# Optimization experiments

Measured on AMD Instinct MI355X. Metric: run time of the kernel, lower is better.

The kernel has to match this reference:

```python
import jax, jax.numpy as jnp
import numpy as np

N = 8192          # total samples = n_ways * num_instances
D = 512           # embedding dim
NUM_INSTANCES = 8 # shots per class
MARGIN = 0.3
W = 1.0
EPS = 1e-12


def setup_inputs() -> dict:
    key = jax.random.key(0)
    inputs = jax.random.normal(key, (N, D), dtype=jnp.float32)
    # targets[i] = class id; classes are contiguous blocks of NUM_INSTANCES
    targets = jnp.arange(N, dtype=jnp.int32) // NUM_INSTANCES
    return {"inputs": inputs, "targets": targets}


def _pairwise_euclid(a, b):
    # sqrt(clamp(||a||^2 + ||b||^2 - 2 a.b, eps)) -- same as torch addmm path
    sq_a = jnp.sum(a * a, axis=1)          # [na]
    sq_b = jnp.sum(b * b, axis=1)          # [nb]
    d2 = sq_a[:, None] + sq_b[None, :] - 2.0 * (a @ b.T)
    return jnp.sqrt(jnp.clip(d2, EPS, None))


def reference(inputs, targets):
    n = inputs.shape[0]
    n_ways = n // NUM_INSTANCES

    dist = _pairwise_euclid(inputs, inputs)              # [n, n]
    mask = targets[:, None] == targets[None, :]          # same-class mask

    # batch-hard mining: hardest positive (max same-class dist),
    # hardest negative (min different-class dist), fully vectorized
    dist_ap = jnp.max(jnp.where(mask, dist, -jnp.inf), axis=1)  # [n]
    dist_an = jnp.min(jnp.where(mask, jnp.inf, dist), axis=1)   # [n]

    # MarginRankingLoss with y=1: mean(relu(-(dist_an - dist_ap) + margin))
    loss = jnp.mean(jax.nn.relu(dist_ap - dist_an + MARGIN))

    dist_p = jnp.mean(dist_ap)
    dist_n = jnp.mean(dist_an)

    # prototype accuracy
    protos = inputs.reshape(n_ways, NUM_INSTANCES, -1).mean(axis=1)  # [n_ways, D]
    logits = _pairwise_euclid(inputs, protos)                        # [n, n_ways]
    estimate = jnp.argmin(logits, axis=1)
    labels = jnp.arange(n_ways, dtype=estimate.dtype).repeat(NUM_INSTANCES)
    acc = jnp.mean((estimate == labels).astype(jnp.float32))

    return (W * loss, acc, dist_p, dist_n)
```

## Files before the change

### kernel.cpp

```cpp
#include <hip/hip_runtime.h>
#include <hip/hip_bf16.h>
#include <stdint.h>

#define NTOT  8192
#define DIM   512
#define NI    8
#define NWAYS 1024
#define TILE  128
#define BK    64
#define NSYM  2080
#define NBLK  2592
#define MARGINV 0.3f

typedef float f32x4 __attribute__((ext_vector_type(4)));

__device__ __forceinline__ unsigned f2o(float f) {
  unsigned u = __float_as_uint(f);
  return (u & 0x80000000u) ? ~u : (u | 0x80000000u);
}
__device__ __forceinline__ float o2f(unsigned u) {
  u = (u & 0x80000000u) ? (u & 0x7fffffffu) : ~u;
  return __uint_as_float(u);
}

__device__ __forceinline__ float wave_sum64(float v) {
#pragma unroll
  for (int s = 32; s; s >>= 1) v += __shfl_xor(v, s, 64);
  return v;
}

__device__ __forceinline__ void async_ld16(const void* g, void* l) {
  __builtin_amdgcn_global_load_lds(
      (__attribute__((address_space(1))) void*)(uintptr_t)g,
      (__attribute__((address_space(3))) void*)l, 16, 0, 0);
}

__global__ __launch_bounds__(256) void prep(
    const float* __restrict__ A, float* __restrict__ sq,
    float* __restrict__ psq, unsigned char* __restrict__ A8,
    unsigned char* __restrict__ P8,
    unsigned long long* __restrict__ an_key,
    unsigned long long* __restrict__ ap_key,
    unsigned long long* __restrict__ pr_key) {
  const int w = threadIdx.x >> 6;
  const int l = threadIdx.x & 63;
  const int b = blockIdx.x;
  if (b < NTOT / 4) {
    const int row = b * 4 + w;
    const float4* rp = (const float4*)(A + (size_t)row * DIM);
    unsigned* op = (unsigned*)(A8 + (size_t)row * DIM);
    float s = 0.f;
#pragma unroll
    for (int m = 0; m < 2; ++m) {
      const float4 v = rp[l + 64 * m];
      s = fmaf(v.x, v.x, fmaf(v.y, v.y, fmaf(v.z, v.z, fmaf(v.w, v.w, s))));
      int wd = 0;
      wd = __builtin_amdgcn_cvt_pk_fp8_f32(v.x, v.y, wd, false);
      wd = __builtin_amdgcn_cvt_pk_fp8_f32(v.z, v.w, wd, true);
      op[l + 64 * m] = (unsigned)wd;
    }
    s = wave_sum64(s);
    if (l == 0) {
      sq[row] = s;
      an_key[row] = ~0ull;
      pr_key[row] = ~0ull;
      ap_key[row] = 0ull;
    }
  } else {
    const int c = (b - NTOT / 4) * 4 + w;
    unsigned* op = (unsigned*)(P8 + (size_t)c * DIM);
    float s = 0.f;
#pragma unroll
    for (int m = 0; m < 2; ++m) {
      float4 p = {0.f, 0.f, 0.f, 0.f};
#pragma unroll
      for (int r = 0; r < NI; ++r) {
        const float4 v =
            ((const float4*)(A + (size_t)(c * NI + r) * DIM))[l + 64 * m];
        p.x += v.x; p.y += v.y; p.z += v.z; p.w += v.w;
      }
      p.x *= (1.f / NI); p.y *= (1.f / NI); p.z *= (1.f / NI); p.w *= (1.f / NI);
      s = fmaf(p.x, p.x, fmaf(p.y, p.y, fmaf(p.z, p.z, fmaf(p.w, p.w, s))));
      int wd = 0;
      wd = __builtin_amdgcn_cvt_pk_fp8_f32(p.x, p.y, wd, false);
      wd = __builtin_amdgcn_cvt_pk_fp8_f32(p.z, p.w, wd, true);
      op[l + 64 * m] = (unsigned)wd;
    }
    s = wave_sum64(s);
    if (l == 0) psq[c] = s;
  }
}

__global__ __launch_bounds__(256) void gemm_fused(
    const unsigned char* __restrict__ A, const unsigned char* __restrict__ P,
    const float* __restrict__ sq, const float* __restrict__ psq,
    unsigned long long* __restrict__ an_key,
    unsigned long long* __restrict__ ap_key,
    unsigned long long* __restrict__ pr_key) {
  __shared__ __align__(16) unsigned char As[2][TILE * BK];
  __shared__ __align__(16) unsigned char Bs[2][TILE * BK];
  __shared__ unsigned long long rowkey[TILE][2];
  __shared__ unsigned long long sidekey[TILE][2];

  const int braw = blockIdx.x;
  const int b = (braw & 7) * (NBLK / 8) + (braw >> 3);
  const bool isProto = b >= NSYM;
  int bi, bj;
  const unsigned char* Bmat;
  const float* sqB;
  if (!isProto) {
    int rem = b, Si = 0, Sj = 0;
    for (;;) {
      const int cnt = (Si == Sj) ? 36 : 64;
      if (rem < cnt) break;
      rem -= cnt;
      ++Si;
      if (Si > Sj) { Si = 0; ++Sj; }
    }
    int bi_l, bj_l;
    if (Si == Sj) {
      bj_l = 0;
      while ((bj_l + 1) * (bj_l + 2) / 2 <= rem) ++bj_l;
      bi_l = rem - bj_l * (bj_l + 1) / 2;
    } else {
      bi_l = rem & 7;
      bj_l = rem >> 3;
    }
    bi = Si * 8 + bi_l;
    bj = Sj * 8 + bj_l;
    Bmat = A;
    sqB = sq;
  } else {
    const int p = b - NSYM;
    bj = p & 7;
    bi = p >> 3;
    Bmat = P;
    sqB = psq;
  }
  const int rowBase = bi * TILE;
  const int colBase = bj * TILE;
  const bool isDiag = !isProto && (bi == bj);
  const bool colSide = !isProto && (bi != bj);

  const int t = threadIdx.x;
  const int lane = t & 63;
  const int wv = t >> 6;
  const int wr = wv >> 1;
  const int wc = wv & 1;
  const int quad = lane >> 4;
  const int lc = lane & 15;
  const int s_lc = (lc & 3) ^ ((lc >> 2) & 3);
  const int koff0 = (((quad >> 1) ^ s_lc) * 16) + (quad & 1) * 8;
  const int koff1 = (((2 + (quad >> 1)) ^ s_lc) * 16) + (quad & 1) * 8;

  const int strow = wv * 16 + (lane >> 2);
  const int s_st = ((lane >> 2) & 3) ^ ((lane >> 4) & 3);
  const int ucol = ((lane & 3) ^ s_st) * 16;
  const unsigned char* gA = A + (size_t)(rowBase + strow) * DIM + ucol;
  const unsigned char* gB = Bmat + (size_t)(colBase + strow) * DIM + ucol;
  const int ldsOff = wv * 1024 + lane * 16;

  f32x4 acc[4][4] = {};

#pragma unroll
  for (int rd = 0; rd < 2; ++rd) {
    async_ld16(gA + rd * 32768, &As[0][rd * 4096 + ldsOff]);
    async_ld16(gB + rd * 32768, &Bs[0][rd * 4096 + ldsOff]);
  }
  __syncthreads();

  int rowA[4], rowB[4];
#pragma unroll
  for (int x = 0; x < 4; ++x) {
    rowA[x] = (wr * 64 + x * 16 + lc) * BK;
    rowB[x] = (wc * 64 + x * 16 + lc) * BK;
  }

  int cur = 0;
  for (int kt = 0; kt < DIM; kt += BK) {
    const int nxt = cur ^ 1;
    if (kt + BK < DIM) {
#pragma unroll
      for (int rd = 0; rd < 2; ++rd) {
        async_ld16(gA + rd * 32768 + kt + BK, &As[nxt][rd * 4096 + ldsOff]);
        async_ld16(gB + rd * 32768 + kt + BK, &Bs[nxt][rd * 4096 + ldsOff]);
      }
    }
#pragma unroll
    for (int kk = 0; kk < 2; ++kk) {
      const int ko = kk ? koff1 : koff0;
      long af[4], bfr[4];
#pragma unroll
      for (int x = 0; x < 4; ++x) {
        af[x]  = *(const long*)(&As[cur][rowA[x] + ko]);
        bfr[x] = *(const long*)(&Bs[cur][rowB[x] + ko]);
      }
#pragma unroll
      for (int x = 0; x < 4; ++x)
#pragma unroll
        for (int y = 0; y < 4; ++y)
          acc[x][y] = __builtin_amdgcn_mfma_f32_16x16x32_fp8_fp8(
              af[x], bfr[y], acc[x][y], 0, 0, 0);
    }
    __syncthreads();
    cur = nxt;
  }

  float sb[4];
#pragma unroll
  for (int y = 0; y < 4; ++y) sb[y] = sqB[colBase + wc * 64 + y * 16 + lc];

  const float INF = __int_as_float(0x7f800000);

#pragma unroll
  for (int x = 0; x < 4; ++x) {
    unsigned long long kmin[4] = {~0ull, ~0ull, ~0ull, ~0ull};
    unsigned long long kmax[4] = {0ull, 0ull, 0ull, 0ull};
#pragma unroll
    for (int y = 0; y < 4; ++y) {
      const int col = colBase + wc * 64 + y * 16 + lc;
#pragma unroll
      for (int r = 0; r < 4; ++r) {
        const float v = fmaf(-2.f, acc[x][y][r], sb[y]);
        if (isDiag) {
          const int row = rowBase + wr * 64 + x * 16 + quad * 4 + r;
          const bool same = (row >> 3) == (col >> 3);
          const unsigned long long kn =
              ((unsigned long long)f2o(same ? INF : v) << 32) | (unsigned)col;
          const unsigned long long kx =
              ((unsigned long long)f2o(same ? v : -INF) << 32) | (unsigned)col;
          if (kn < kmin[r]) kmin[r] = kn;
          if (kx > kmax[r]) kmax[r] = kx;
        } else {
          const unsigned long long kn =
              ((unsigned long long)f2o(v) << 32) | (unsigned)col;
          if (kn < kmin[r]) kmin[r] = kn;
        }
      }
    }
#pragma unroll
    for (int r = 0; r < 4; ++r) {
#pragma unroll
      for (int s = 1; s < 16; s <<= 1) {
        const unsigned long long o = __shfl_xor(kmin[r], s, 64);
        if (o < kmin[r]) kmin[r] = o;
      }
    }
    if (isDiag) {
#pragma unroll
      for (int r = 0; r < 4; ++r) {
#pragma unroll
        for (int s = 1; s < 16; s <<= 1) {
          const unsigned long long o = __shfl_xor(kmax[r], s, 64);
          if (o > kmax[r]) kmax[r] = o;
        }
      }
    }
    if (lc == 0) {
#pragma unroll
      for (int r = 0; r < 4; ++r) {
        rowkey[wr * 64 + x * 16 + quad * 4 + r][wc] = kmin[r];
        if (isDiag) sidekey[wr * 64 + x * 16 + quad * 4 + r][wc] = kmax[r];
      }
    }
  }

  if (colSide) {
    float sa[4][4];
#pragma unroll
    for (int x = 0; x < 4; ++x)
#pragma unroll
      for (int r = 0; r < 4; ++r)
        sa[x][r] = sq[rowBase + wr * 64 + x * 16 + quad * 4 + r];
#pragma unroll
    for (int y = 0; y < 4; ++y) {
      unsigned long long kc = ~0ull;
#pragma unroll
      for (int x = 0; x < 4; ++x)
#pragma unroll
        for (int r = 0; r < 4; ++r) {
          const int row = rowBase + wr * 64 + x * 16 + quad * 4 + r;
          const float v = fmaf(-2.f, acc[x][y][r], sa[x][r]);
          const unsigned long long k =
              ((unsigned long long)f2o(v) << 32) | (unsigned)row;
          if (k < kc) kc = k;
        }
#pragma unroll
      for (int s = 16; s < 64; s <<= 1) {
        const unsigned long long o = __shfl_xor(kc, s, 64);
        if (o < kc) kc = o;
      }
      if (quad == 0) sidekey[wc * 64 + y * 16 + lc][wr] = kc;
    }
  }

  __syncthreads();
  if (t < TILE) {
    unsigned long long a = rowkey[t][0];
    const unsigned long long c = rowkey[t][1];
    if (c < a) a = c;
    atomicMin((isProto ? pr_key : an_key) + rowBase + t, a);
  } else if (t < 2 * TILE) {
    const int i = t - TILE;
    if (colSide) {
      unsigned long long a = sidekey[i][0];
      const unsigned long long c = sidekey[i][1];
      if (c < a) a = c;
      atomicMin(an_key + colBase + i, a);
    } else if (isDiag) {
      unsigned long long a = sidekey[i][0];
      const unsigned long long c = sidekey[i][1];
      if (c > a) a = c;
      atomicMax(ap_key + rowBase + i, a);
    }
  }
}

__global__ void finalize_kernel(const float* __restrict__ sq,
                                const unsigned long long* __restrict__ an_key,
                                const unsigned long long* __restrict__ ap_key,
                                const unsigned long long* __restrict__ pr_key,
                                float* __restrict__ out) {
  const int tid = threadIdx.x;
  float loss = 0.f, sp = 0.f, sn = 0.f, acc = 0.f;
#pragma unroll
  for (int i = tid; i < NTOT; i += 1024) {
    const float s = sq[i];
    const float ap = sqrtf(fmaxf(s + o2f((unsigned)(ap_key[i] >> 32)), 1e-12f));
    const float an = sqrtf(fmaxf(s + o2f((unsigned)(an_key[i] >> 32)), 1e-12f));
    loss += fmaxf(ap - an + MARGINV, 0.f);
    sp += ap;
    sn += an;
    acc += ((unsigned)(pr_key[i] & 0xffffffffu) == (unsigned)(i >> 3)) ? 1.f : 0.f;
  }
  loss = wave_sum64(loss);
  sp = wave_sum64(sp);
  sn = wave_sum64(sn);
  acc = wave_sum64(acc);
  __shared__ float red[16][4];
  const int w = tid >> 6, l = tid & 63;
  if (l == 0) { red[w][0] = loss; red[w][1] = acc; red[w][2] = sp; red[w][3] = sn; }
  __syncthreads();
  if (tid == 0) {
    float L = 0, Ac = 0, Pm = 0, Nn = 0;
    for (int i = 0; i < 16; ++i) {
      L += red[i][0]; Ac += red[i][1]; Pm += red[i][2]; Nn += red[i][3];
    }
    out[0] = L / NTOT;
    out[1] = Ac / NTOT;
    out[2] = Pm / NTOT;
    out[3] = Nn / NTOT;
  }
}

extern "C" void kernel_launch(void* const* d_in, const int* in_sizes, int n_in,
                              void* d_out, int out_size, void* d_ws, size_t ws_size,
                              hipStream_t stream) {
  const float* inputs = (const float*)d_in[0];
  float* out = (float*)d_out;
  char* w = (char*)d_ws;
  float* sq  = (float*)(w);
  float* psq = (float*)(w + 32768);
  unsigned long long* an_key = (unsigned long long*)(w + 36864);
  unsigned long long* ap_key = (unsigned long long*)(w + 102400);
  unsigned long long* pr_key = (unsigned long long*)(w + 167936);
  unsigned char* A8 = (unsigned char*)(w + 233472);
  unsigned char* P8 = (unsigned char*)(w + 233472 + (size_t)NTOT * DIM);

  prep<<<NTOT / 4 + NWAYS / 4, 256, 0, stream>>>(inputs, sq, psq, A8, P8,
                                                 an_key, ap_key, pr_key);
  gemm_fused<<<NBLK, 256, 0, stream>>>(A8, P8, sq, psq,
                                       an_key, ap_key, pr_key);
  finalize_kernel<<<1, 1024, 0, stream>>>(sq, an_key, ap_key, pr_key, out);
}
```

Measured before the change: 161.2 us.

## Double K tile to 128 and use 32-bit value-only LDS atomics for mining

Doubles the K tile of the fp8 MFMA GEMM to 128 and rewrites the LDS load mapping and XOR swizzle to match, which halves the K iterations and barriers per block. For the triplet mining path it drops the 64-bit (value, index) keys. Per-row and per-column minima and maxima are now reduced in registers and merged through 32-bit LDS atomics, replacing the shuffle trees, and 32-bit global atomics replace the 64-bit ones. LDS use per block roughly doubles (about 64KB for tiles), which may reduce occupancy, and the LDS atomics add contention.

Result: faster. 135.0 us (-16.2%).

```diff
diff --git a/kernel.cpp b/kernel.cpp
--- a/kernel.cpp
+++ b/kernel.cpp
@@ -7,7 +7,7 @@
 #define NI    8
 #define NWAYS 1024
 #define TILE  128
-#define BK    64
+#define BK    128
 #define NSYM  2080
 #define NBLK  2592
 #define MARGINV 0.3f
@@ -39,8 +39,7 @@
     const float* __restrict__ A, float* __restrict__ sq,
     float* __restrict__ psq, unsigned char* __restrict__ A8,
     unsigned char* __restrict__ P8,
-    unsigned long long* __restrict__ an_key,
-    unsigned long long* __restrict__ ap_key,
+    unsigned* __restrict__ an_u32, unsigned* __restrict__ ap_u32,
     unsigned long long* __restrict__ pr_key) {
   const int w = threadIdx.x >> 6;
   const int l = threadIdx.x & 63;
@@ -62,9 +61,9 @@
     s = wave_sum64(s);
     if (l == 0) {
       sq[row] = s;
-      an_key[row] = ~0ull;
+      an_u32[row] = ~0u;
+      ap_u32[row] = 0u;
       pr_key[row] = ~0ull;
-      ap_key[row] = 0ull;
     }
   } else {
     const int c = (b - NTOT / 4) * 4 + w;
@@ -94,13 +93,14 @@
 __global__ __launch_bounds__(256) void gemm_fused(
     const unsigned char* __restrict__ A, const unsigned char* __restrict__ P,
     const float* __restrict__ sq, const float* __restrict__ psq,
-    unsigned long long* __restrict__ an_key,
-    unsigned long long* __restrict__ ap_key,
+    unsigned* __restrict__ an_u32, unsigned* __restrict__ ap_u32,
     unsigned long long* __restrict__ pr_key) {
   __shared__ __align__(16) unsigned char As[2][TILE * BK];
   __shared__ __align__(16) unsigned char Bs[2][TILE * BK];
+  __shared__ unsigned rmin[TILE];
+  __shared__ unsigned cmin[TILE];
+  __shared__ unsigned amax[TILE];
   __shared__ unsigned long long rowkey[TILE][2];
-  __shared__ unsigned long long sidekey[TILE][2];
 
   const int braw = blockIdx.x;
   const int b = (braw & 7) * (NBLK / 8) + (braw >> 3);
@@ -149,25 +149,13 @@
   const int wc = wv & 1;
   const int quad = lane >> 4;
   const int lc = lane & 15;
-  const int s_lc = (lc & 3) ^ ((lc >> 2) & 3);
-  const int koff0 = (((quad >> 1) ^ s_lc) * 16) + (quad & 1) * 8;
-  const int koff1 = (((2 + (quad >> 1)) ^ s_lc) * 16) + (quad & 1) * 8;
-
-  const int strow = wv * 16 + (lane >> 2);
-  const int s_st = ((lane >> 2) & 3) ^ ((lane >> 4) & 3);
-  const int ucol = ((lane & 3) ^ s_st) * 16;
-  const unsigned char* gA = A + (size_t)(rowBase + strow) * DIM + ucol;
-  const unsigned char* gB = Bmat + (size_t)(colBase + strow) * DIM + ucol;
-  const int ldsOff = wv * 1024 + lane * 16;
-
-  f32x4 acc[4][4] = {};
-
-#pragma unroll
-  for (int rd = 0; rd < 2; ++rd) {
-    async_ld16(gA + rd * 32768, &As[0][rd * 4096 + ldsOff]);
-    async_ld16(gB + rd * 32768, &Bs[0][rd * 4096 + ldsOff]);
-  }
-  __syncthreads();
+
+  if (t < TILE) { rmin[t] = ~0u; cmin[t] = ~0u; amax[t] = 0u; }
+
+  int koff[4];
+#pragma unroll
+  for (int c = 0; c < 4; ++c)
+    koff[c] = (((c * 2 + (quad >> 1)) ^ (lc & 7)) * 16) + (quad & 1) * 8;
 
   int rowA[4], rowB[4];
 #pragma unroll
@@ -176,24 +164,44 @@
     rowB[x] = (wc * 64 + x * 16 + lc) * BK;
   }
 
-  int cur = 0;
-  for (int kt = 0; kt < DIM; kt += BK) {
+  const int l8 = lane >> 3;
+  const int ul = ((lane & 7) ^ (l8 & 7)) * 16;
+  const unsigned char* gA = A + (size_t)(rowBase + l8) * DIM + ul;
+  const unsigned char* gB = Bmat + (size_t)(colBase + l8) * DIM + ul;
+  const int ldsL = lane * 16;
+
+  f32x4 acc[4][4] = {};
+
+#pragma unroll
+  for (int j = 0; j < 4; ++j) {
+    const int rr = wv * 4 + j;
+    async_ld16(gA + (size_t)rr * 8 * DIM, &As[0][rr * 1024 + ldsL]);
+    async_ld16(gB + (size_t)rr * 8 * DIM, &Bs[0][rr * 1024 + ldsL]);
+  }
+  __syncthreads();
+
+#pragma unroll
+  for (int it = 0; it < 4; ++it) {
+    const int cur = it & 1;
     const int nxt = cur ^ 1;
-    if (kt + BK < DIM) {
-#pragma unroll
-      for (int rd = 0; rd < 2; ++rd) {
-        async_ld16(gA + rd * 32768 + kt + BK, &As[nxt][rd * 4096 + ldsOff]);
-        async_ld16(gB + rd * 32768 + kt + BK, &Bs[nxt][rd * 4096 + ldsOff]);
-      }
-    }
-#pragma unroll
-    for (int kk = 0; kk < 2; ++kk) {
-      const int ko = kk ? koff1 : koff0;
+    const int kt = it * BK;
+    if (it < 3) {
+#pragma unroll
+      for (int j = 0; j < 4; ++j) {
+        const int rr = wv * 4 + j;
+        async_ld16(gA + (size_t)rr * 8 * DIM + kt + BK, &As[nxt][rr * 1024 + ldsL]);
+        async_ld16(gB + (size_t)rr * 8 * DIM + kt + BK, &Bs[nxt][rr * 1024 + ldsL]);
+      }
+    }
+    const unsigned char* Ac = &As[cur][0];
+    const unsigned char* Bc = &Bs[cur][0];
+#pragma unroll
+    for (int c = 0; c < 4; ++c) {
       long af[4], bfr[4];
 #pragma unroll
       for (int x = 0; x < 4; ++x) {
-        af[x]  = *(const long*)(&As[cur][rowA[x] + ko]);
-        bfr[x] = *(const long*)(&Bs[cur][rowB[x] + ko]);
+        af[x]  = *(const long*)(Ac + rowA[x] + koff[c]);
+        bfr[x] = *(const long*)(Bc + rowB[x] + koff[c]);
       }
 #pragma unroll
       for (int x = 0; x < 4; ++x)
@@ -203,7 +211,6 @@
               af[x], bfr[y], acc[x][y], 0, 0, 0);
     }
     __syncthreads();
-    cur = nxt;
   }
 
   float sb[4];
@@ -212,113 +219,100 @@
 
   const float INF = __int_as_float(0x7f800000);
 
-#pragma unroll
-  for (int x = 0; x < 4; ++x) {
-    unsigned long long kmin[4] = {~0ull, ~0ull, ~0ull, ~0ull};
-    unsigned long long kmax[4] = {0ull, 0ull, 0ull, 0ull};
-#pragma unroll
-    for (int y = 0; y < 4; ++y) {
-      const int col = colBase + wc * 64 + y * 16 + lc;
+  if (!isProto) {
+#pragma unroll
+    for (int x = 0; x < 4; ++x) {
 #pragma unroll
       for (int r = 0; r < 4; ++r) {
-        const float v = fmaf(-2.f, acc[x][y][r], sb[y]);
-        if (isDiag) {
-          const int row = rowBase + wr * 64 + x * 16 + quad * 4 + r;
-          const bool same = (row >> 3) == (col >> 3);
-          const unsigned long long kn =
-              ((unsigned long long)f2o(same ? INF : v) << 32) | (unsigned)col;
-          const unsigned long long kx =
-              ((unsigned long long)f2o(same ? v : -INF) << 32) | (unsigned)col;
-          if (kn < kmin[r]) kmin[r] = kn;
-          if (kx > kmax[r]) kmax[r] = kx;
-        } else {
+        const int row = rowBase + wr * 64 + x * 16 + quad * 4 + r;
+        float mv = INF, mx = -INF;
+#pragma unroll
+        for (int y = 0; y < 4; ++y) {
+          const float v = fmaf(-2.f, acc[x][y][r], sb[y]);
+          if (isDiag) {
+            const int col = colBase + wc * 64 + y * 16 + lc;
+            const bool same = (row >> 3) == (col >> 3);
+            mv = fminf(mv, same ? INF : v);
+            mx = fmaxf(mx, same ? v : -INF);
+          } else {
+            mv = fminf(mv, v);
+          }
+        }
+        atomicMin(&rmin[row - rowBase], f2o(mv));
+        if (isDiag) atomicMax(&amax[row - rowBase], f2o(mx));
+      }
+    }
+    if (colSide) {
+      float sa[4][4];
+#pragma unroll
+      for (int x = 0; x < 4; ++x)
+#pragma unroll
+        for (int r = 0; r < 4; ++r)
+          sa[x][r] = sq[rowBase + wr * 64 + x * 16 + quad * 4 + r];
+#pragma unroll
+      for (int y = 0; y < 4; ++y) {
+        float cv = INF;
+#pragma unroll
+        for (int x = 0; x < 4; ++x)
+#pragma unroll
+          for (int r = 0; r < 4; ++r)
+            cv = fminf(cv, fmaf(-2.f, acc[x][y][r], sa[x][r]));
+        atomicMin(&cmin[wc * 64 + y * 16 + lc], f2o(cv));
+      }
+    }
+  } else {
+#pragma unroll
+    for (int x = 0; x < 4; ++x) {
+      unsigned long long kmin[4] = {~0ull, ~0ull, ~0ull, ~0ull};
+#pragma unroll
+      for (int y = 0; y < 4; ++y) {
+        const int col = colBase + wc * 64 + y * 16 + lc;
+#pragma unroll
+        for (int r = 0; r < 4; ++r) {
+          const float v = fmaf(-2.f, acc[x][y][r], sb[y]);
           const unsigned long long kn =
               ((unsigned long long)f2o(v) << 32) | (unsigned)col;
           if (kn < kmin[r]) kmin[r] = kn;
         }
       }
-    }
-#pragma unroll
-    for (int r = 0; r < 4; ++r) {
-#pragma unroll
-      for (int s = 1; s < 16; s <<= 1) {
-        const unsigned long long o = __shfl_xor(kmin[r], s, 64);
-        if (o < kmin[r]) kmin[r] = o;
-      }
-    }
-    if (isDiag) {
 #pragma unroll
       for (int r = 0; r < 4; ++r) {
 #pragma unroll
         for (int s = 1; s < 16; s <<= 1) {
-          const unsigned long long o = __shfl_xor(kmax[r], s, 64);
-          if (o > kmax[r]) kmax[r] = o;
+          const unsigned long long o = __shfl_xor(kmin[r], s, 64);
+          if (o < kmin[r]) kmin[r] = o;
         }
       }
-    }
-    if (lc == 0) {
-#pragma unroll
-      for (int r = 0; r < 4; ++r) {
-        rowkey[wr * 64 + x * 16 + quad * 4 + r][wc] = kmin[r];
-        if (isDiag) sidekey[wr * 64 + x * 16 + quad * 4 + r][wc] = kmax[r];
-      }
-    }
-  }
-
-  if (colSide) {
-    float sa[4][4];
-#pragma unroll
-    for (int x = 0; x < 4; ++x)
-#pragma unroll
-      for (int r = 0; r < 4; ++r)
-        sa[x][r] = sq[rowBase + wr * 64 + x * 16 + quad * 4 + r];
-#pragma unroll
-    for (int y = 0; y < 4; ++y) {
-      unsigned long long kc = ~0ull;
-#pragma unroll
-      for (int x = 0; x < 4; ++x)
-#pragma unroll
-        for (int r = 0; r < 4; ++r) {
-          const int row = rowBase + wr * 64 + x * 16 + quad * 4 + r;
-          const float v = fmaf(-2.f, acc[x][y][r], sa[x][r]);
-          const unsigned long long k =
-              ((unsigned long long)f2o(v) << 32) | (unsigned)row;
-          if (k < kc) kc = k;
-        }
-#pragma unroll
-      for (int s = 16; s < 64; s <<= 1) {
-        const unsigned long long o = __shfl_xor(kc, s, 64);
-        if (o < kc) kc = o;
-      }
-      if (quad == 0) sidekey[wc * 64 + y * 16 + lc][wr] = kc;
+      if (lc == 0) {
+#pragma unroll
+        for (int r = 0; r < 4; ++r)
+          rowkey[wr * 64 + x * 16 + quad * 4 + r][wc] = kmin[r];
+      }
     }
   }
 
   __syncthreads();
-  if (t < TILE) {
-    unsigned long long a = rowkey[t][0];
-    const unsigned long long c = rowkey[t][1];
-    if (c < a) a = c;
-    atomicMin((isProto ? pr_key : an_key) + rowBase + t, a);
-  } else if (t < 2 * TILE) {
-    const int i = t - TILE;
-    if (colSide) {
-      unsigned long long a = sidekey[i][0];
-      const unsigned long long c = sidekey[i][1];
+  if (isProto) {
+    if (t < TILE) {
+      unsigned long long a = rowkey[t][0];
+      const unsigned long long c = rowkey[t][1];
       if (c < a) a = c;
-      atomicMin(an_key + colBase + i, a);
-    } else if (isDiag) {
-      unsigned long long a = sidekey[i][0];
-      const unsigned long long c = sidekey[i][1];
-      if (c > a) a = c;
-      atomicMax(ap_key + rowBase + i, a);
+      atomicMin(pr_key + rowBase + t, a);
+    }
+  } else {
+    if (t < TILE) {
+      atomicMin(an_u32 + rowBase + t, rmin[t]);
+    } else if (t < 2 * TILE) {
+      const int i = t - TILE;
+      if (colSide) atomicMin(an_u32 + colBase + i, cmin[i]);
+      else if (isDiag) atomicMax(ap_u32 + rowBase + i, amax[i]);
     }
   }
 }
 
 __global__ void finalize_kernel(const float* __restrict__ sq,
-                                const unsigned long long* __restrict__ an_key,
-                                const unsigned long long* __restrict__ ap_key,
+                                const unsigned* __restrict__ an_u32,
+                                const unsigned* __restrict__ ap_u32,
                                 const unsigned long long* __restrict__ pr_key,
                                 float* __restrict__ out) {
   const int tid = threadIdx.x;
@@ -326,8 +320,8 @@
 #pragma unroll
   for (int i = tid; i < NTOT; i += 1024) {
     const float s = sq[i];
-    const float ap = sqrtf(fmaxf(s + o2f((unsigned)(ap_key[i] >> 32)), 1e-12f));
-    const float an = sqrtf(fmaxf(s + o2f((unsigned)(an_key[i] >> 32)), 1e-12f));
+    const float ap = sqrtf(fmaxf(s + o2f(ap_u32[i]), 1e-12f));
+    const float an = sqrtf(fmaxf(s + o2f(an_u32[i]), 1e-12f));
     loss += fmaxf(ap - an + MARGINV, 0.f);
     sp += ap;
     sn += an;
@@ -361,15 +355,15 @@
   char* w = (char*)d_ws;
   float* sq  = (float*)(w);
   float* psq = (float*)(w + 32768);
-  unsigned long long* an_key = (unsigned long long*)(w + 36864);
-  unsigned long long* ap_key = (unsigned long long*)(w + 102400);
-  unsigned long long* pr_key = (unsigned long long*)(w + 167936);
-  unsigned char* A8 = (unsigned char*)(w + 233472);
-  unsigned char* P8 = (unsigned char*)(w + 233472 + (size_t)NTOT * DIM);
+  unsigned* an_u32 = (unsigned*)(w + 36864);
+  unsigned* ap_u32 = (unsigned*)(w + 69632);
+  unsigned long long* pr_key = (unsigned long long*)(w + 102400);
+  unsigned char* A8 = (unsigned char*)(w + 167936);
+  unsigned char* P8 = (unsigned char*)(w + 167936 + (size_t)NTOT * DIM);
 
   prep<<<NTOT / 4 + NWAYS / 4, 256, 0, stream>>>(inputs, sq, psq, A8, P8,
-                                                 an_key, ap_key, pr_key);
+                                                 an_u32, ap_u32, pr_key);
   gemm_fused<<<NBLK, 256, 0, stream>>>(A8, P8, sq, psq,
-                                       an_key, ap_key, pr_key);
-  finalize_kernel<<<1, 1024, 0, stream>>>(sq, an_key, ap_key, pr_key, out);
-}
+                                       an_u32, ap_u32, pr_key);
+  finalize_kernel<<<1, 1024, 0, stream>>>(sq, an_u32, ap_u32, pr_key, out);
+}
```
